# Kernel tuning notes

Measured on AMD Instinct MI355X. Metric: run time of the kernel, lower is better.

## Reference

```python
import jax, jax.numpy as jnp
import numpy as np

N_NODES = 100000
N_EDGES = 3200000
D_IN = 256
D_OUT = 256


def setup_inputs() -> dict:
    key = jax.random.key(0)
    k1, k2, k3, k4, k5 = jax.random.split(key, 5)
    x = jax.random.normal(k1, (N_NODES, D_IN), dtype=jnp.float32)
    weight = jax.random.normal(k2, (D_IN, D_OUT), dtype=jnp.float32)
    edge_rows = jax.random.randint(k3, (N_EDGES,), 0, N_NODES, dtype=jnp.int32)
    edge_cols = jax.random.randint(k4, (N_EDGES,), 0, N_NODES, dtype=jnp.int32)
    edge_vals = jax.random.uniform(k5, (N_EDGES,), dtype=jnp.float32)
    return {"x": x, "weight": weight, "edge_rows": edge_rows,
            "edge_cols": edge_cols, "edge_vals": edge_vals}


def reference(x, weight, edge_rows, edge_cols, edge_vals):
    # GraphConvolution forward (eval mode, dense features, no bias):
    #   xw  = x @ W                      [N, D_OUT]
    #   out = relu(A_sparse @ xw)        A given as COO edge list
    xw = x @ weight  # [N, D_OUT]
    msgs = edge_vals[:, None] * xw[edge_cols]  # gather source features, scale
    agg = jax.ops.segment_sum(msgs, edge_rows, num_segments=N_NODES)
    return jax.nn.relu(agg)
```

## Files before the change

kernel.cpp:

```cpp
#include <hip/hip_runtime.h>
#include <hip/hip_bf16.h>

#define N_NODES 100000
#define N_EDGES 3200000
#define D 256

#define RSH3 6
#define RPB3 64
#define NB3 ((N_NODES + RPB3 - 1) / RPB3)
#define FILL_CH 8192
#define NBLK_F ((N_EDGES + FILL_CH - 1) / FILL_CH)
#define CLOC_W (NB3 + 1)
#define RCAP 12
#define SCAP 3072
#define OCAP 64

typedef __attribute__((ext_vector_type(8))) short short8;
typedef __attribute__((ext_vector_type(4))) float floatx4;

__device__ __forceinline__ unsigned short f32_to_bf16_rne(float f) {
    unsigned int u = __float_as_uint(f);
    u += 0x7FFFu + ((u >> 16) & 1u);
    return (unsigned short)(u >> 16);
}
__device__ __forceinline__ float bf16_bits_to_f32(unsigned short b) {
    return __uint_as_float(((unsigned int)b) << 16);
}
__device__ __forceinline__ float blo(unsigned int x) { return __uint_as_float(x << 16); }
__device__ __forceinline__ float bhi(unsigned int x) { return __uint_as_float(x & 0xFFFF0000u); }

__global__ __launch_bounds__(256) void convert_w_k(const float* __restrict__ w,
                                                   unsigned short* __restrict__ wsw) {
    int t = blockIdx.x * 256 + threadIdx.x;
    int j     = t & 7;
    int lane  = (t >> 3) & 63;
    int kstep = (t >> 9) & 7;
    int ntile = t >> 12;
    int k = kstep * 32 + (lane >> 4) * 8 + j;
    int n = ntile * 16 + (lane & 15);
    wsw[t] = f32_to_bf16_rne(w[k * D + n]);
}

__global__ __launch_bounds__(512) void gemm_xw_k(const float* __restrict__ x,
                                                 const unsigned short* __restrict__ wsw,
                                                 unsigned short* __restrict__ xwb) {
    __shared__ uint4 wlds[8192];
    const int tid = threadIdx.x;
#pragma unroll
    for (int i = 0; i < 16; ++i) {
        int idx = i * 512 + tid;
        wlds[idx] = ((const uint4*)wsw)[idx];
    }
    __syncthreads();

    const int lane = tid & 63;
    const int wave = tid >> 6;
    const int q    = lane >> 4;
    const int ml   = lane & 15;
    const long rowBase = (long)blockIdx.x * 128 + wave * 16;
    long arow = rowBase + ml;
    if (arow >= N_NODES) arow = 0;
    const float* xr = x + arow * (long)D;

    floatx4 acc[16];
#pragma unroll
    for (int i = 0; i < 16; ++i) acc[i] = (floatx4){0.f, 0.f, 0.f, 0.f};

    const short8* wfrag = (const short8*)wlds;

#pragma unroll
    for (int ks = 0; ks < 8; ++ks) {
        const float4 a0 = *(const float4*)(xr + ks * 32 + q * 8);
        const float4 a1 = *(const float4*)(xr + ks * 32 + q * 8 + 4);
        short8 af;
        af[0] = (short)f32_to_bf16_rne(a0.x);
        af[1] = (short)f32_to_bf16_rne(a0.y);
        af[2] = (short)f32_to_bf16_rne(a0.z);
        af[3] = (short)f32_to_bf16_rne(a0.w);
        af[4] = (short)f32_to_bf16_rne(a1.x);
        af[5] = (short)f32_to_bf16_rne(a1.y);
        af[6] = (short)f32_to_bf16_rne(a1.z);
        af[7] = (short)f32_to_bf16_rne(a1.w);
#pragma unroll
        for (int nt = 0; nt < 16; ++nt) {
            acc[nt] = __builtin_amdgcn_mfma_f32_16x16x32_bf16(
                af, wfrag[(nt * 8 + ks) * 64 + lane], acc[nt], 0, 0, 0);
        }
    }

#pragma unroll
    for (int nt = 0; nt < 16; ++nt) {
#pragma unroll
        for (int r = 0; r < 4; ++r) {
            long orow = rowBase + q * 4 + r;
            if (orow < N_NODES)
                xwb[orow * (long)D + nt * 16 + ml] = f32_to_bf16_rne(acc[nt][r]);
        }
    }
}

__global__ __launch_bounds__(512) void bfill_k(const int* __restrict__ erow,
                                               const int* __restrict__ ecol,
                                               const float* __restrict__ eval,
                                               int* __restrict__ Cloc,
                                               unsigned long long* __restrict__ recs) {
    __shared__ unsigned long long lrec[FILL_CH];
    __shared__ int h[NB3];
    __shared__ int cur[NB3];
    __shared__ int wsum[8];
    const int tid = threadIdx.x;
    const int blk = blockIdx.x;
    const int s = blk * FILL_CH;
    const int e = min(s + FILL_CH, N_EDGES);
    const int n = e - s;

    for (int i = tid; i < NB3; i += 512) h[i] = 0;
    __syncthreads();

    for (int i = s + tid; i < e; i += 512) atomicAdd(&h[erow[i] >> RSH3], 1);
    __syncthreads();

    {
        const int b0 = 4 * tid;
        int v0 = (b0     < NB3) ? h[b0]     : 0;
        int v1 = (b0 + 1 < NB3) ? h[b0 + 1] : 0;
        int v2 = (b0 + 2 < NB3) ? h[b0 + 2] : 0;
        int v3 = (b0 + 3 < NB3) ? h[b0 + 3] : 0;
        int s4 = v0 + v1 + v2 + v3;
        const int lane = tid & 63;
        const int wv = tid >> 6;
        int x = s4;
#pragma unroll
        for (int d = 1; d < 64; d <<= 1) {
            int u = __shfl_up(x, d);
            if (lane >= d) x += u;
        }
        if (lane == 63) wsum[wv] = x;
        __syncthreads();
        if (wv == 0) {
            int y = (lane < 8) ? wsum[lane] : 0;
#pragma unroll
            for (int d = 1; d < 8; d <<= 1) {
                int u = __shfl_up(y, d);
                if (lane >= d) y += u;
            }
            if (lane < 8) wsum[lane] = y;
        }
        __syncthreads();
        int excl = x - s4 + ((wv > 0) ? wsum[wv - 1] : 0);
        int* crow = Cloc + (size_t)blk * CLOC_W;
        if (b0     < NB3) { cur[b0]     = excl;                crow[b0]     = excl; }
        if (b0 + 1 < NB3) { cur[b0 + 1] = excl + v0;           crow[b0 + 1] = excl + v0; }
        if (b0 + 2 < NB3) { cur[b0 + 2] = excl + v0 + v1;      crow[b0 + 2] = excl + v0 + v1; }
        if (b0 + 3 < NB3) { cur[b0 + 3] = excl + v0 + v1 + v2; crow[b0 + 3] = excl + v0 + v1 + v2; }
        if (tid == 0) crow[NB3] = n;
    }
    __syncthreads();

    for (int i = s + tid; i < e; i += 512) {
        int r = erow[i];
        int b = r >> RSH3;
        unsigned long long rec =
            ((unsigned long long)(r & (RPB3 - 1)) << 33) |
            ((unsigned long long)f32_to_bf16_rne(eval[i]) << 17) |
            (unsigned int)ecol[i];
        int pos = atomicAdd(&cur[b], 1);
        lrec[pos] = rec;
    }
    __syncthreads();

    unsigned long long* grow = recs + (size_t)blk * FILL_CH;
    for (int i = tid; i < n; i += 512) grow[i] = lrec[i];
}

__device__ __forceinline__ unsigned long long fetch_rec(
    const unsigned long long* __restrict__ recs,
    const unsigned short* __restrict__ S,
    const unsigned short* __restrict__ P, int i) {
    int lo = 0, hi = NBLK_F;
#pragma unroll
    for (int it = 0; it < 9; ++it) {
        int mid = (lo + hi) >> 1;
        if ((int)P[mid] <= i) lo = mid; else hi = mid;
    }
    return recs[(size_t)lo * FILL_CH + (int)S[lo] + (i - (int)P[lo])];
}

__global__ __launch_bounds__(256) void baggr_k(const unsigned short* __restrict__ xwb,
                                               const int* __restrict__ Cloc,
                                               const unsigned long long* __restrict__ recs,
                                               float* __restrict__ out) {
    __shared__ unsigned int   cols[SCAP];
    __shared__ unsigned short vals[SCAP];
    __shared__ unsigned long long ovfl[OCAP];
    __shared__ unsigned short S[NBLK_F];
    __shared__ unsigned short L[NBLK_F];
    __shared__ unsigned short P[NBLK_F + 1];
    __shared__ int hist[RPB3];
    __shared__ int cur[RPB3];
    __shared__ int wsum4[4];
    __shared__ int novf;
    const int t = threadIdx.x;
    const int b = blockIdx.x;

    if (t < RPB3) hist[t] = 0;
    if (t == 0) novf = 0;
    for (int j = t; j < NBLK_F; j += 256) {
        const int* crow = Cloc + (size_t)j * CLOC_W + b;
        int a = crow[0], c = crow[1];
        S[j] = (unsigned short)a;
        L[j] = (unsigned short)(c - a);
    }
    __syncthreads();

    {
        const int j0 = 2 * t, j1 = 2 * t + 1;
        int v0 = (j0 < NBLK_F) ? (int)L[j0] : 0;
        int v1 = (j1 < NBLK_F) ? (int)L[j1] : 0;
        int sv = v0 + v1;
        const int lane = t & 63;
        const int wv = t >> 6;
        int x = sv;
#pragma unroll
        for (int d = 1; d < 64; d <<= 1) {
            int u = __shfl_up(x, d);
            if (lane >= d) x += u;
        }
        if (lane == 63) wsum4[wv] = x;
        __syncthreads();
        if (wv == 0) {
            int y = (lane < 4) ? wsum4[lane] : 0;
#pragma unroll
            for (int d = 1; d < 4; d <<= 1) {
                int u = __shfl_up(y, d);
                if (lane >= d) y += u;
            }
            if (lane < 4) wsum4[lane] = y;
        }
        __syncthreads();
        int excl = x - sv + ((wv > 0) ? wsum4[wv - 1] : 0);
        if (j0 < NBLK_F) P[j0] = (unsigned short)excl;
        if (j1 < NBLK_F) P[j1] = (unsigned short)(excl + v0);
        if (j0 == NBLK_F - 1) P[NBLK_F] = (unsigned short)(excl + v0);
        if (j1 == NBLK_F - 1) P[NBLK_F] = (unsigned short)(excl + v0 + v1);
    }
    __syncthreads();
    const int nfull = (int)P[NBLK_F];

    unsigned long long myrec[RCAP];
#pragma unroll
    for (int k = 0; k < RCAP; ++k) {
        int i = k * 256 + t;
        if (i < nfull) myrec[k] = fetch_rec(recs, S, P, i);
    }
#pragma unroll
    for (int k = 0; k < RCAP; ++k) {
        int i = k * 256 + t;
        if (i < nfull) atomicAdd(&hist[(int)((myrec[k] >> 33) & 63u)], 1);
    }
    for (int i = SCAP + t; i < nfull; i += 256)
        atomicAdd(&hist[(int)((fetch_rec(recs, S, P, i) >> 33) & 63u)], 1);
    __syncthreads();

    if (t < 64) {
        int v = hist[t];
        int x = v;
#pragma unroll
        for (int d = 1; d < 64; d <<= 1) {
            int u = __shfl_up(x, d);
            if (t >= d) x += u;
        }
        cur[t] = x - v;
    }
    __syncthreads();

#pragma unroll
    for (int k = 0; k < RCAP; ++k) {
        int i = k * 256 + t;
        if (i < nfull) {
            unsigned long long rec = myrec[k];
            int rl = (int)((rec >> 33) & 63u);
            int pos = atomicAdd(&cur[rl], 1);
            if (pos < SCAP) {
                cols[pos] = (unsigned int)(rec & 0x1FFFFu);
                vals[pos] = (unsigned short)((rec >> 17) & 0xFFFFu);
            } else {
                int o = atomicAdd(&novf, 1);
                if (o < OCAP) ovfl[o] = rec;
            }
        }
    }
    for (int i = SCAP + t; i < nfull; i += 256) {
        unsigned long long rec = fetch_rec(recs, S, P, i);
        int rl = (int)((rec >> 33) & 63u);
        int pos = atomicAdd(&cur[rl], 1);
        if (pos < SCAP) {
            cols[pos] = (unsigned int)(rec & 0x1FFFFu);
            vals[pos] = (unsigned short)((rec >> 17) & 0xFFFFu);
        } else {
            int o = atomicAdd(&novf, 1);
            if (o < OCAP) ovfl[o] = rec;
        }
    }
    __syncthreads();

    const int wave = t >> 6;
    const int lane = t & 63;
    const int half = lane >> 5;
    const int hl   = lane & 31;
    const int nov  = min(novf, OCAP);

#pragma unroll 1
    for (int rr = 0; rr < 16; ++rr) {
        const int rl = wave * 16 + rr;
        const int r = (b << RSH3) + rl;
        if (r >= N_NODES) break;
        const int e_ = cur[rl];
        const int s_ = e_ - hist[rl];
        const int e = min(e_, SCAP);
        const int s = min(s_, SCAP);

        float acc[8];
#pragma unroll
        for (int k = 0; k < 8; ++k) acc[k] = 0.f;

#pragma unroll 1
        for (int jb = s; jb < e; jb += 64) {
            const int cnt = min(64, e - jb);
            const int pairs = (cnt + 1) >> 1;
            const int hp = cnt >> 1;
            int tt = 0;

#define FMA8(qv, bv)                                                           \
            acc[0] += bv * blo(qv.x); acc[1] += bv * bhi(qv.x);                \
            acc[2] += bv * blo(qv.y); acc[3] += bv * bhi(qv.y);                \
            acc[4] += bv * blo(qv.z); acc[5] += bv * bhi(qv.z);                \
            acc[6] += bv * blo(qv.w); acc[7] += bv * bhi(qv.w);
#define SLOTL(ss, qv, bv)                                                      \
            {                                                                  \
                int src = jb + 2 * (tt + (ss)) + half;                         \
                unsigned int bc = cols[src];                                   \
                bv = bf16_bits_to_f32(vals[src]);                              \
                qv = ((const uint4*)(xwb + (size_t)bc * D))[hl];               \
            }

#pragma unroll 1
            for (; tt + 8 <= hp; tt += 8) {
                uint4 q0, q1, q2, q3, q4, q5, q6, q7;
                float b0, b1, b2, b3, b4, b5, b6, b7;
                SLOTL(0, q0, b0) SLOTL(1, q1, b1) SLOTL(2, q2, b2) SLOTL(3, q3, b3)
                SLOTL(4, q4, b4) SLOTL(5, q5, b5) SLOTL(6, q6, b6) SLOTL(7, q7, b7)
                FMA8(q0, b0) FMA8(q1, b1) FMA8(q2, b2) FMA8(q3, b3)
                FMA8(q4, b4) FMA8(q5, b5) FMA8(q6, b6) FMA8(q7, b7)
            }
            if (tt + 4 <= hp) {
                uint4 q0, q1, q2, q3;
                float b0, b1, b2, b3;
                SLOTL(0, q0, b0) SLOTL(1, q1, b1) SLOTL(2, q2, b2) SLOTL(3, q3, b3)
                FMA8(q0, b0) FMA8(q1, b1) FMA8(q2, b2) FMA8(q3, b3)
                tt += 4;
            }
#undef SLOTL
#pragma unroll 1
            for (; tt < pairs; ++tt) {
                int src = jb + 2 * tt + half;
                int srcc = min(src, e - 1);
                unsigned int bc = cols[srcc];
                float vv = bf16_bits_to_f32(vals[srcc]);
                float bv = (src < e) ? vv : 0.f;
                uint4 q = ((const uint4*)(xwb + (size_t)bc * D))[hl];
                FMA8(q, bv)
            }
        }

#pragma unroll 1
        for (int k = 0; k < nov; ++k) {
            unsigned long long rec = ovfl[k];
            if ((int)((rec >> 33) & 63u) == rl) {
                unsigned int bc = (unsigned int)(rec & 0x1FFFFu);
                float vv = bf16_bits_to_f32((unsigned short)((rec >> 17) & 0xFFFFu));
                float bv = (half == 0) ? vv : 0.f;
                uint4 q = ((const uint4*)(xwb + (size_t)bc * D))[hl];
                FMA8(q, bv)
            }
        }
#undef FMA8

#pragma unroll
        for (int k = 0; k < 8; ++k) acc[k] += __shfl_xor(acc[k], 32);

        const int sl = lane >> 1;
        const int par = lane & 1;
        float4 o;
        {
            float a0 = __shfl(acc[0], sl), c0 = __shfl(acc[4], sl);
            float a1 = __shfl(acc[1], sl), c1 = __shfl(acc[5], sl);
            float a2 = __shfl(acc[2], sl), c2 = __shfl(acc[6], sl);
            float a3 = __shfl(acc[3], sl), c3 = __shfl(acc[7], sl);
            o.x = par ? c0 : a0;
            o.y = par ? c1 : a1;
            o.z = par ? c2 : a2;
            o.w = par ? c3 : a3;
        }
        o.x = fmaxf(o.x, 0.f);
        o.y = fmaxf(o.y, 0.f);
        o.z = fmaxf(o.z, 0.f);
        o.w = fmaxf(o.w, 0.f);
        ((float4*)(out + (size_t)r * D))[lane] = o;
    }
}

extern "C" void kernel_launch(void* const* d_in, const int* in_sizes, int n_in,
                              void* d_out, int out_size, void* d_ws, size_t ws_size,
                              hipStream_t stream) {
    const float* x    = (const float*)d_in[0];
    const float* w    = (const float*)d_in[1];
    const int*   erow = (const int*)d_in[2];
    const int*   ecol = (const int*)d_in[3];
    const float* eval = (const float*)d_in[4];
    float* out = (float*)d_out;

    char* p = (char*)d_ws;
    auto align = [](size_t v) { return (v + 255) & ~(size_t)255; };

    unsigned short* xwb = (unsigned short*)p;
    p += align((size_t)N_NODES * D * sizeof(unsigned short));
    unsigned short* wsw = (unsigned short*)p;
    p += align((size_t)D * D * sizeof(unsigned short));
    int* Cloc = (int*)p;
    p += align((size_t)NBLK_F * CLOC_W * sizeof(int));
    unsigned long long* recs = (unsigned long long*)p;
    p += align((size_t)NBLK_F * FILL_CH * sizeof(unsigned long long));

    convert_w_k<<<(D * D) / 256, 256, 0, stream>>>(w, wsw);
    gemm_xw_k<<<(N_NODES + 127) / 128, 512, 0, stream>>>(x, wsw, xwb);
    bfill_k<<<NBLK_F, 512, 0, stream>>>(erow, ecol, eval, Cloc, recs);
    baggr_k<<<NB3, 256, 0, stream>>>(xwb, Cloc, recs, out);
}
```

Baseline: 491.6 us.

## Transpose bucket offset table and scatter fill records directly to global

Adds a tiled transpose kernel that converts the per-fill-block bucket offset table into a bucket-major 16-bit layout, so each aggregation block reads its start/end offsets contiguously instead of with a large stride. The fill kernel also drops its 64KB shared staging buffer and writes each record straight to its global slot, which frees LDS for occupancy but makes the global writes scattered within a block's 64KB region. It adds one extra kernel launch and a small extra buffer.

```diff
diff --git a/kernel.cpp b/kernel.cpp
--- a/kernel.cpp
+++ b/kernel.cpp
@@ -104,7 +104,6 @@
                                                const float* __restrict__ eval,
                                                int* __restrict__ Cloc,
                                                unsigned long long* __restrict__ recs) {
-    __shared__ unsigned long long lrec[FILL_CH];
     __shared__ int h[NB3];
     __shared__ int cur[NB3];
     __shared__ int wsum[8];
@@ -157,6 +156,7 @@
     }
     __syncthreads();
 
+    unsigned long long* grow = recs + (size_t)blk * FILL_CH;
     for (int i = s + tid; i < e; i += 512) {
         int r = erow[i];
         int b = r >> RSH3;
@@ -165,12 +165,36 @@
             ((unsigned long long)f32_to_bf16_rne(eval[i]) << 17) |
             (unsigned int)ecol[i];
         int pos = atomicAdd(&cur[b], 1);
-        lrec[pos] = rec;
-    }
-    __syncthreads();
-
-    unsigned long long* grow = recs + (size_t)blk * FILL_CH;
-    for (int i = tid; i < n; i += 512) grow[i] = lrec[i];
+        grow[pos] = rec;
+    }
+}
+
+#define TRT_B ((CLOC_W + 63) / 64)
+#define TRT_K ((NBLK_F + 63) / 64)
+__global__ __launch_bounds__(256) void tr_k(const int* __restrict__ Cloc,
+                                            unsigned short* __restrict__ Ctr) {
+    __shared__ unsigned short tile[64][65];
+    const int bt = blockIdx.x % TRT_B;
+    const int kt = blockIdx.x / TRT_B;
+#pragma unroll
+    for (int i = 0; i < 16; ++i) {
+        int r = i * 4 + (threadIdx.x >> 6);
+        int c = threadIdx.x & 63;
+        int blk = kt * 64 + r;
+        int b   = bt * 64 + c;
+        tile[r][c] = (blk < NBLK_F && b < CLOC_W)
+                         ? (unsigned short)Cloc[(size_t)blk * CLOC_W + b] : (unsigned short)0;
+    }
+    __syncthreads();
+#pragma unroll
+    for (int i = 0; i < 16; ++i) {
+        int r = i * 4 + (threadIdx.x >> 6);
+        int c = threadIdx.x & 63;
+        int b   = bt * 64 + r;
+        int blk = kt * 64 + c;
+        if (b < CLOC_W && blk < NBLK_F)
+            Ctr[(size_t)b * NBLK_F + blk] = tile[c][r];
+    }
 }
 
 __device__ __forceinline__ unsigned long long fetch_rec(
@@ -187,7 +211,7 @@
 }
 
 __global__ __launch_bounds__(256) void baggr_k(const unsigned short* __restrict__ xwb,
-                                               const int* __restrict__ Cloc,
+                                               const unsigned short* __restrict__ Ctr,
                                                const unsigned long long* __restrict__ recs,
                                                float* __restrict__ out) {
     __shared__ unsigned int   cols[SCAP];
@@ -205,11 +229,14 @@
 
     if (t < RPB3) hist[t] = 0;
     if (t == 0) novf = 0;
-    for (int j = t; j < NBLK_F; j += 256) {
-        const int* crow = Cloc + (size_t)j * CLOC_W + b;
-        int a = crow[0], c = crow[1];
-        S[j] = (unsigned short)a;
-        L[j] = (unsigned short)(c - a);
+    {
+        const unsigned short* Sb = Ctr + (size_t)b * NBLK_F;
+        const unsigned short* Eb = Ctr + (size_t)(b + 1) * NBLK_F;
+        for (int j = t; j < NBLK_F; j += 256) {
+            unsigned short a = Sb[j];
+            S[j] = a;
+            L[j] = (unsigned short)(Eb[j] - a);
+        }
     }
     __syncthreads();
 
@@ -429,11 +456,14 @@
     p += align((size_t)D * D * sizeof(unsigned short));
     int* Cloc = (int*)p;
     p += align((size_t)NBLK_F * CLOC_W * sizeof(int));
+    unsigned short* Ctr = (unsigned short*)p;
+    p += align((size_t)CLOC_W * NBLK_F * sizeof(unsigned short));
     unsigned long long* recs = (unsigned long long*)p;
     p += align((size_t)NBLK_F * FILL_CH * sizeof(unsigned long long));
 
     convert_w_k<<<(D * D) / 256, 256, 0, stream>>>(w, wsw);
     gemm_xw_k<<<(N_NODES + 127) / 128, 512, 0, stream>>>(x, wsw, xwb);
     bfill_k<<<NBLK_F, 512, 0, stream>>>(erow, ecol, eval, Cloc, recs);
-    baggr_k<<<NB3, 256, 0, stream>>>(xwb, Cloc, recs, out);
-}
+    tr_k<<<TRT_B * TRT_K, 256, 0, stream>>>(Cloc, Ctr);
+    baggr_k<<<NB3, 256, 0, stream>>>(xwb, Ctr, recs, out);
+}
```

New measurement: 540.1 us. +9.9%, slower.
